# Kernel optimization log

Hardware: AMD Instinct MI355X
Metric: run time of the kernel (lower is better)

Reference implementation:

```python
import jax, jax.numpy as jnp
import numpy as np

TEMPERATURE = 0.07
B, D = 8192, 1024
NUM_CLASSES = 100


def setup_inputs() -> dict:
    key = jax.random.key(0)
    k1, k2 = jax.random.split(key)
    e = jax.random.normal(k1, (B, D), dtype=jnp.float32)
    e = e / jnp.linalg.norm(e, axis=1, keepdims=True)  # module assumes L2-normalized embeds
    labels = jax.random.randint(k2, (B,), 0, NUM_CLASSES)
    return {"embeds": e, "labels": labels}


def reference(embeds, labels):
    # logits[i, j] = <e_i, e_j> / T    (B, B)
    logits = (embeds @ embeds.T) / TEMPERATURE
    same = labels[None, :] == labels[:, None]  # (B, B) symmetric label-match mask
    # denominator: logsumexp over rows i with a DIFFERENT label than column j
    neg_masked = jnp.where(same, -jnp.inf, logits)
    base_denom_row = jax.scipy.special.logsumexp(neg_masked, axis=0)  # (B,)
    # numerator pairs: same label, off-diagonal
    in_numer = same & ~jnp.eye(B, dtype=bool)
    numer_count = in_numer.sum(axis=0)  # (B,) per-column positive count
    # log_denom[i, j] = logaddexp(logits[i, j], base_denom_row[i]) where in_numer
    log_denom = jnp.logaddexp(logits, base_denom_row[:, None])
    ce = jnp.where(in_numer, log_denom - logits, 0.0)  # -(numer - log_denom), 0 elsewhere
    count_safe = jnp.maximum(numer_count, 1).astype(ce.dtype)  # guard (unused cols are all-zero)
    return jnp.sum(ce / count_safe[None, :]) / B
```

## Files before the change

### kernel.cpp

```cpp
#include <hip/hip_runtime.h>
#include <math.h>

#define B 8192
#define D 1024
#define INV_T (1.0f/0.07f)
#define CMAX (1.0f/0.07f)
#define SPLITS 8
#define CW (B/SPLITS)
#define MAXM 256
#define NCLS 100
#define NRB (B/128)
#define NTRI (NRB*(NRB+1)/2)

typedef __attribute__((ext_vector_type(4))) float  f32x4;
typedef __attribute__((ext_vector_type(8))) int    i32x8;

__device__ __forceinline__ int sw02(int x) {
    return (x & 2) | ((x & 1) << 2) | ((x >> 2) & 1);
}

__global__ __launch_bounds__(256) void convert_kernel(const float* __restrict__ E,
                                                      unsigned char* __restrict__ E8) {
    int i = blockIdx.x * 256 + threadIdx.x;
    float4 v = ((const float4*)E)[i];
    int lo = __builtin_amdgcn_cvt_pk_fp8_f32(v.x, v.y, 0, false);
    int pk = __builtin_amdgcn_cvt_pk_fp8_f32(v.z, v.w, lo, true);
    ((int*)E8)[i] = pk;
}

__device__ __forceinline__ void stage_tile8(const unsigned char* __restrict__ E8,
                                            char* As, char* Bs,
                                            int row0, int col0, int k0,
                                            int w, int srow, int sk) {
#pragma unroll
    for (int q = 0; q < 4; ++q) {
        const char* ga = (const char*)(E8 + (size_t)(row0 + srow + q * 8) * D + k0) + sk;
        const char* gb = (const char*)(E8 + (size_t)(col0 + srow + q * 8) * D + k0) + sk;
        __builtin_amdgcn_global_load_lds(
            (const __attribute__((address_space(1))) unsigned int*)ga,
            (__attribute__((address_space(3))) unsigned int*)(As + w * 4096 + q * 1024),
            16, 0, 0);
        __builtin_amdgcn_global_load_lds(
            (const __attribute__((address_space(1))) unsigned int*)gb,
            (__attribute__((address_space(3))) unsigned int*)(Bs + w * 4096 + q * 1024),
            16, 0, 0);
    }
}

__global__ __launch_bounds__(256, 2) void lse_sym_kernel(const unsigned char* __restrict__ E8,
                                                         const int* __restrict__ labels,
                                                         float* __restrict__ part) {
    __shared__ char As[128 * 128];
    __shared__ char Bs[128 * 128];
    __shared__ float sh_r[4][64];
    __shared__ float sh_c[4][64];

    int bid = (blockIdx.x & 7) * (NTRI / 8) + (blockIdx.x >> 3);
    int rb = 0, off = 0;
    while (off + (NRB - rb) <= bid) { off += NRB - rb; ++rb; }
    const int cb = rb + (bid - off);

    const int row0 = rb * 128;
    const int col0 = cb * 128;
    const int t    = threadIdx.x;
    const int lane = t & 63;
    const int w    = t >> 6;
    const int wr   = w >> 1;
    const int wc   = w & 1;

    int rlab[16];
#pragma unroll
    for (int m = 0; m < 4; ++m)
#pragma unroll
        for (int r = 0; r < 4; ++r)
            rlab[m * 4 + r] = labels[row0 + wr * 64 + m * 16 + ((lane >> 4) << 2) + r];
    int clab[4];
#pragma unroll
    for (int n = 0; n < 4; ++n) clab[n] = labels[col0 + wc * 64 + n * 16 + (lane & 15)];

    const int srow = w * 32 + (lane >> 3);
    const int sk   = sw02((lane & 7) ^ (lane >> 3)) << 4;
    const int p    = lane >> 4;
    const int kq   = 2 * (p & 1) + (p >> 1);
    const int swz  = (lane & 7) << 4;
    const int loff = (kq << 4) ^ swz;

    f32x4 acc[4][4];
#pragma unroll
    for (int m = 0; m < 4; ++m)
#pragma unroll
        for (int n = 0; n < 4; ++n) { f32x4 z = {0.f, 0.f, 0.f, 0.f}; acc[m][n] = z; }

    const int nt = D / 128;
    for (int kt = 0; kt < nt; ++kt) {
        __syncthreads();
        stage_tile8(E8, As, Bs, row0, col0, kt * 128, w, srow, sk);
        __syncthreads();

        i32x8 b[4];
#pragma unroll
        for (int n = 0; n < 4; ++n) {
            int row = wc * 64 + n * 16 + (lane & 15);
            const char* pb = Bs + row * 128;
            int4 lo = *(const int4*)(pb + loff);
            int4 hi = *(const int4*)(pb + (loff ^ 64));
            b[n][0] = lo.x; b[n][1] = lo.y; b[n][2] = lo.z; b[n][3] = lo.w;
            b[n][4] = hi.x; b[n][5] = hi.y; b[n][6] = hi.z; b[n][7] = hi.w;
        }

        __builtin_amdgcn_s_setprio(1);
#pragma unroll
        for (int m = 0; m < 4; ++m) {
            int row = wr * 64 + m * 16 + (lane & 15);
            const char* pa = As + row * 128;
            int4 lo = *(const int4*)(pa + loff);
            int4 hi = *(const int4*)(pa + (loff ^ 64));
            i32x8 a;
            a[0] = lo.x; a[1] = lo.y; a[2] = lo.z; a[3] = lo.w;
            a[4] = hi.x; a[5] = hi.y; a[6] = hi.z; a[7] = hi.w;
#pragma unroll
            for (int n = 0; n < 4; ++n)
                acc[m][n] = __builtin_amdgcn_mfma_scale_f32_16x16x128_f8f6f4(
                    a, b[n], acc[m][n], 0, 0, 0, 127, 0, 127);
        }
        __builtin_amdgcn_s_setprio(0);
    }

    float rsum[16];
#pragma unroll
    for (int i = 0; i < 16; ++i) rsum[i] = 0.f;
    float csum[4];
#pragma unroll
    for (int n = 0; n < 4; ++n) csum[n] = 0.f;

#pragma unroll
    for (int m = 0; m < 4; ++m)
#pragma unroll
        for (int n = 0; n < 4; ++n)
#pragma unroll
            for (int r = 0; r < 4; ++r) {
                float x = acc[m][n][r] * INV_T;
                float e = (rlab[m * 4 + r] != clab[n]) ? __expf(x - CMAX) : 0.f;
                rsum[m * 4 + r] += e;
                csum[n] += e;
            }

#pragma unroll
    for (int o = 1; o < 16; o <<= 1)
#pragma unroll
        for (int i = 0; i < 16; ++i) rsum[i] += __shfl_xor(rsum[i], o);
    if ((lane & 15) == 0) {
#pragma unroll
        for (int m = 0; m < 4; ++m)
#pragma unroll
            for (int r = 0; r < 4; ++r)
                sh_r[w][m * 16 + ((lane >> 4) << 2) + r] = rsum[m * 4 + r];
    }
#pragma unroll
    for (int n = 0; n < 4; ++n) {
        csum[n] += __shfl_xor(csum[n], 16);
        csum[n] += __shfl_xor(csum[n], 32);
    }
    if (lane < 16) {
#pragma unroll
        for (int n = 0; n < 4; ++n) sh_c[w][n * 16 + lane] = csum[n];
    }
    __syncthreads();
    if (t < 128) {
        int wri = t >> 6, idx = t & 63;
        float s = sh_r[wri * 2][idx] + sh_r[wri * 2 + 1][idx];
        part[(size_t)(row0 + t) * NRB + cb] = s;
    } else if (rb != cb) {
        int c = t - 128;
        int wci = c >> 6, idx = c & 63;
        float s = sh_c[wci][idx] + sh_c[2 + wci][idx];
        part[(size_t)(col0 + c) * NRB + rb] = s;
    }
}

__global__ __launch_bounds__(256) void combine_kernel(const float* __restrict__ part,
                                                      float* __restrict__ base) {
    int i = blockIdx.x * 256 + threadIdx.x;
    float s = 0.f;
#pragma unroll
    for (int k = 0; k < NRB; ++k) s += part[(size_t)i * NRB + k];
    base[i] = logf(s) + CMAX;
}

__global__ __launch_bounds__(256) void class_list_kernel(const int* __restrict__ labels,
                                                         int* __restrict__ members,
                                                         int* __restrict__ cnt) {
    const int c = blockIdx.x;
    const int tt = threadIdx.x;
    const int lane = tt & 63, w = tt >> 6;
    __shared__ int wcnt[4];
    int cw = 0;
    for (int b0 = w * 2048; b0 < (w + 1) * 2048; b0 += 64)
        cw += __popcll(__ballot(labels[b0 + lane] == c));
    if (lane == 0) wcnt[w] = cw;
    __syncthreads();
    int cum = 0;
    for (int x = 0; x < w; ++x) cum += wcnt[x];
    for (int b0 = w * 2048; b0 < (w + 1) * 2048; b0 += 64) {
        bool match = (labels[b0 + lane] == c);
        unsigned long long mask = __ballot(match);
        int pre = __popcll(mask & ((1ull << lane) - 1ull));
        if (match) members[c * MAXM + cum + pre] = b0 + lane;
        cum += __popcll(mask);
    }
    if (tt == 0) cnt[c] = wcnt[0] + wcnt[1] + wcnt[2] + wcnt[3];
}

__global__ __launch_bounds__(256) void numer_mfma_kernel(const unsigned char* __restrict__ E8,
                                                         const float* __restrict__ base,
                                                         const int* __restrict__ members,
                                                         const int* __restrict__ cnt,
                                                         float* __restrict__ part2) {
    const int c  = blockIdx.x;
    const int rt = blockIdx.y;
    const int ctile = blockIdx.z;
    const int t    = threadIdx.x;
    const int lane = t & 63;
    const int w    = t >> 6;
    const int n    = cnt[c];
    const int pidx = c * 16 + rt * 4 + ctile;

    __shared__ char As[64 * 128];
    __shared__ char Bs[64 * 128];
    __shared__ float red[256];

    if (rt * 64 >= n || ctile * 64 >= n) {
        if (t == 0) part2[pidx] = 0.f;
        return;
    }

    int gi[4]; float bi[4]; bool iv[4];
#pragma unroll
    for (int r = 0; r < 4; ++r) {
        int il = rt * 64 + w * 16 + ((lane >> 4) << 2) + r;
        iv[r] = (il < n);
        int idx = members[c * MAXM + (iv[r] ? il : 0)];
        gi[r] = il;
        bi[r] = base[idx];
    }
    int gj[4]; bool jv[4];
#pragma unroll
    for (int nn = 0; nn < 4; ++nn) {
        int jl = ctile * 64 + nn * 16 + (lane & 15);
        jv[nn] = (jl < n);
        gj[nn] = jl;
    }

    const int lr   = (lane >> 3);
    const int sk   = sw02((lane & 7) ^ lr) << 4;
    const int pp   = lane >> 4;
    const int kq   = 2 * (pp & 1) + (pp >> 1);
    const int swz  = (lane & 7) << 4;
    const int loff = (kq << 4) ^ swz;

    int arow[2], brow[2];
#pragma unroll
    for (int q = 0; q < 2; ++q) {
        int al = rt * 64 + w * 16 + q * 8 + lr;
        int bl = ctile * 64 + w * 16 + q * 8 + lr;
        arow[q] = members[c * MAXM + ((al < n) ? al : 0)];
        brow[q] = members[c * MAXM + ((bl < n) ? bl : 0)];
    }

    f32x4 acc[4];
#pragma unroll
    for (int nn = 0; nn < 4; ++nn) { f32x4 z = {0.f, 0.f, 0.f, 0.f}; acc[nn] = z; }

    for (int kt = 0; kt < D / 128; ++kt) {
        __syncthreads();
#pragma unroll
        for (int q = 0; q < 2; ++q) {
            const char* ga = (const char*)(E8 + (size_t)arow[q] * D + kt * 128) + sk;
            const char* gb = (const char*)(E8 + (size_t)brow[q] * D + kt * 128) + sk;
            __builtin_amdgcn_global_load_lds(
                (const __attribute__((address_space(1))) unsigned int*)ga,
                (__attribute__((address_space(3))) unsigned int*)(As + w * 2048 + q * 1024),
                16, 0, 0);
            __builtin_amdgcn_global_load_lds(
                (const __attribute__((address_space(1))) unsigned int*)gb,
                (__attribute__((address_space(3))) unsigned int*)(Bs + w * 2048 + q * 1024),
                16, 0, 0);
        }
        __syncthreads();

        i32x8 a, b[4];
        {
            int row = w * 16 + (lane & 15);
            const char* pa = As + row * 128;
            int4 lo = *(const int4*)(pa + loff);
            int4 hi = *(const int4*)(pa + (loff ^ 64));
            a[0] = lo.x; a[1] = lo.y; a[2] = lo.z; a[3] = lo.w;
            a[4] = hi.x; a[5] = hi.y; a[6] = hi.z; a[7] = hi.w;
        }
#pragma unroll
        for (int nn = 0; nn < 4; ++nn) {
            int row = nn * 16 + (lane & 15);
            const char* pb = Bs + row * 128;
            int4 lo = *(const int4*)(pb + loff);
            int4 hi = *(const int4*)(pb + (loff ^ 64));
            b[nn][0] = lo.x; b[nn][1] = lo.y; b[nn][2] = lo.z; b[nn][3] = lo.w;
            b[nn][4] = hi.x; b[nn][5] = hi.y; b[nn][6] = hi.z; b[nn][7] = hi.w;
        }
#pragma unroll
        for (int nn = 0; nn < 4; ++nn)
            acc[nn] = __builtin_amdgcn_mfma_scale_f32_16x16x128_f8f6f4(
                a, b[nn], acc[nn], 0, 0, 0, 127, 0, 127);
    }

    float psum = 0.f;
#pragma unroll
    for (int nn = 0; nn < 4; ++nn)
#pragma unroll
        for (int r = 0; r < 4; ++r) {
            if (iv[r] && jv[nn] && gi[r] != gj[nn]) {
                float x = bi[r] - acc[nn][r] * INV_T;
                psum += (x > 15.f) ? x : log1pf(__expf(x));
            }
        }
    red[t] = psum;
    __syncthreads();
    for (int g = 128; g > 0; g >>= 1) {
        if (t < g) red[t] += red[t + g];
        __syncthreads();
    }
    if (t == 0) part2[pidx] = red[0];
}

__global__ __launch_bounds__(256) void final2_kernel(const float* __restrict__ part2,
                                                     const int* __restrict__ cnt,
                                                     float* __restrict__ out) {
    __shared__ float red[256];
    int t = threadIdx.x;
    float acc = 0.f;
    for (int p = t; p < NCLS * 16; p += 256) {
        int c = p >> 4;
        float wgt = (cnt[c] > 1) ? 1.f / (float)(cnt[c] - 1) : 0.f;
        acc += part2[p] * wgt;
    }
    red[t] = acc;
    __syncthreads();
    for (int g = 128; g > 0; g >>= 1) {
        if (t < g) red[t] += red[t + g];
        __syncthreads();
    }
    if (t == 0) out[0] = red[0] / (float)B;
}

#define BR 64
#define BC 64
#define KT 32
#define PAD 68
__global__ __launch_bounds__(256) void lse_f32_kernel(const float* __restrict__ E,
                                                      const int* __restrict__ labels,
                                                      float2* __restrict__ part) {
    __shared__ float As[KT][PAD];
    __shared__ float Bs[KT][PAD];
    __shared__ int   clabs[BC];
    __shared__ float msh[BR][16];
    __shared__ float ssh[BR][16];
    const int rb = blockIdx.x, cs = blockIdx.y;
    const int row0 = rb * BR;
    const int t = threadIdx.x;
    const int tx = t & 15, ty = t >> 4;
    int rlab[4];
#pragma unroll
    for (int i = 0; i < 4; ++i) rlab[i] = labels[row0 + ty * 4 + i];
    float m[4], s[4];
#pragma unroll
    for (int i = 0; i < 4; ++i) { m[i] = -INFINITY; s[i] = 0.f; }
    for (int ct = 0; ct < CW / BC; ++ct) {
        const int col0 = cs * CW + ct * BC;
        __syncthreads();
        if (t < BC) clabs[t] = labels[col0 + t];
        float acc[4][4];
#pragma unroll
        for (int i = 0; i < 4; ++i)
#pragma unroll
            for (int j = 0; j < 4; ++j) acc[i][j] = 0.f;
        for (int k0 = 0; k0 < D; k0 += KT) {
            __syncthreads();
#pragma unroll
            for (int q = 0; q < 2; ++q) {
                int id = q * 256 + t, row = id >> 3, kk = (id & 7) * 4;
                float4 va = *(const float4*)&E[(size_t)(row0 + row) * D + k0 + kk];
                As[kk + 0][row] = va.x; As[kk + 1][row] = va.y;
                As[kk + 2][row] = va.z; As[kk + 3][row] = va.w;
                float4 vb = *(const float4*)&E[(size_t)(col0 + row) * D + k0 + kk];
                Bs[kk + 0][row] = vb.x; Bs[kk + 1][row] = vb.y;
                Bs[kk + 2][row] = vb.z; Bs[kk + 3][row] = vb.w;
            }
            __syncthreads();
#pragma unroll
            for (int kk = 0; kk < KT; ++kk) {
                float4 av = *(const float4*)&As[kk][ty * 4];
                float4 bv = *(const float4*)&Bs[kk][tx * 4];
                float a_[4] = {av.x, av.y, av.z, av.w};
                float b_[4] = {bv.x, bv.y, bv.z, bv.w};
#pragma unroll
                for (int i = 0; i < 4; ++i)
#pragma unroll
                    for (int j = 0; j < 4; ++j) acc[i][j] += a_[i] * b_[j];
            }
        }
#pragma unroll
        for (int j = 0; j < 4; ++j) {
            int cl = clabs[tx * 4 + j];
#pragma unroll
            for (int i = 0; i < 4; ++i) {
                if (rlab[i] != cl) {
                    float x = acc[i][j] * INV_T;
                    if (x > m[i]) { s[i] = s[i] * __expf(m[i] - x) + 1.f; m[i] = x; }
                    else           s[i] += __expf(x - m[i]);
                }
            }
        }
    }
    __syncthreads();
#pragma unroll
    for (int i = 0; i < 4; ++i) { msh[ty * 4 + i][tx] = m[i]; ssh[ty * 4 + i][tx] = s[i]; }
    __syncthreads();
    if (t < BR) {
        float M = -INFINITY, S = 0.f;
#pragma unroll
        for (int x = 0; x < 16; ++x) {
            float pm = msh[t][x], ps = ssh[t][x];
            if (pm > M)             { S = S * __expf(M - pm) + ps; M = pm; }
            else if (pm > -INFINITY)  S += ps * __expf(pm - M);
        }
        part[(size_t)(row0 + t) * SPLITS + cs] = make_float2(M, S);
    }
}
__global__ __launch_bounds__(256) void combine_f32_kernel(const float2* __restrict__ part,
                                                          float* __restrict__ base) {
    int i = blockIdx.x * 256 + threadIdx.x;
    if (i >= B) return;
    float M = -INFINITY, S = 0.f;
#pragma unroll
    for (int k = 0; k < SPLITS; ++k) {
        float2 p = part[(size_t)i * SPLITS + k];
        if (p.x > M)             { S = S * __expf(M - p.x) + p.y; M = p.x; }
        else if (p.x > -INFINITY)  S += p.y * __expf(p.x - M);
    }
    base[i] = M + logf(S);
}
__global__ __launch_bounds__(256) void numer_kernel(const float* __restrict__ E,
                                                    const int* __restrict__ labels,
                                                    const float* __restrict__ base,
                                                    const int* __restrict__ members,
                                                    const int* __restrict__ cnt,
                                                    float* __restrict__ rowpart) {
    const int i = blockIdx.x;
    const int t = threadIdx.x;
    const int lane = t & 63, w = t >> 6;
    __shared__ float ei[D];
    __shared__ float wacc[4];
    ((float4*)ei)[t] = ((const float4*)(E + (size_t)i * D))[t];
    const int   li = labels[i];
    const float bi = base[i];
    const int   n  = cnt[li];
    __syncthreads();
    float acc = 0.f;
    const float4* U = (const float4*)ei;
    for (int s = w; s < n; s += 4) {
        int j = members[li * MAXM + s];
        if (j == i) continue;
        const float4* Ej = (const float4*)(E + (size_t)j * D);
        float d = 0.f;
#pragma unroll
        for (int q = 0; q < 4; ++q) {
            float4 v = Ej[lane + 64 * q];
            float4 u = U[lane + 64 * q];
            d += v.x * u.x + v.y * u.y + v.z * u.z + v.w * u.w;
        }
#pragma unroll
        for (int o = 32; o > 0; o >>= 1) d += __shfl_xor(d, o);
        if (lane == 0) {
            float x = bi - d * INV_T;
            acc += (x > 15.f) ? x : log1pf(__expf(x));
        }
    }
    if (lane == 0) wacc[w] = acc;
    __syncthreads();
    if (t == 0) {
        float a = wacc[0] + wacc[1] + wacc[2] + wacc[3];
        rowpart[i] = (n > 1) ? a / (float)(n - 1) : 0.f;
    }
}
__global__ __launch_bounds__(256) void final_kernel(const float* __restrict__ rowpart,
                                                    float* __restrict__ out) {
    __shared__ float red[256];
    int t = threadIdx.x;
    float acc = 0.f;
    for (int k = 0; k < B / 256; ++k) acc += rowpart[t + k * 256];
    red[t] = acc;
    __syncthreads();
    for (int g = 128; g > 0; g >>= 1) {
        if (t < g) red[t] += red[t + g];
        __syncthreads();
    }
    if (t == 0) out[0] = red[0] / (float)B;
}

extern "C" void kernel_launch(void* const* d_in, const int* in_sizes, int n_in,
                              void* d_out, int out_size, void* d_ws, size_t ws_size,
                              hipStream_t stream) {
    const float* E      = (const float*)d_in[0];
    const int*   labels = (const int*)d_in[1];
    float*       out    = (float*)d_out;

    const size_t szE8   = (size_t)B * D;
    const size_t szPart = (size_t)B * NRB * 4;
    const size_t need   = szE8 + szPart + 4 * B + 4 * B + 4 * NCLS * MAXM
                        + 4 * NCLS + 4 * NCLS * 16 + 512;

    if (ws_size >= need) {
        char* ws = (char*)d_ws;
        unsigned char* E8 = (unsigned char*)ws;  ws += szE8;
        float* part    = (float*)ws;   ws += szPart;
        float* base    = (float*)ws;   ws += 4 * B;
        float* rowpart = (float*)ws;   ws += 4 * B;   (void)rowpart;
        int*   members = (int*)ws;     ws += 4 * NCLS * MAXM;
        int*   cnt     = (int*)ws;     ws += 4 * NCLS;
        float* part2   = (float*)ws;

        convert_kernel<<<B * D / 4 / 256, 256, 0, stream>>>(E, E8);
        lse_sym_kernel<<<NTRI, 256, 0, stream>>>(E8, labels, part);
        combine_kernel<<<B / 256, 256, 0, stream>>>(part, base);
        class_list_kernel<<<NCLS, 256, 0, stream>>>(labels, members, cnt);
        numer_mfma_kernel<<<dim3(NCLS, 4, 4), 256, 0, stream>>>(E8, base, members, cnt, part2);
        final2_kernel<<<1, 256, 0, stream>>>(part2, cnt, out);
    } else {
        char* ws = (char*)d_ws;
        float2* part   = (float2*)ws;  ws += sizeof(float2) * B * SPLITS;
        float* base    = (float*)ws;   ws += 4 * B;
        float* rowpart = (float*)ws;   ws += 4 * B;
        int*   members = (int*)ws;     ws += 4 * NCLS * MAXM;
        int*   cnt     = (int*)ws;

        lse_f32_kernel<<<dim3(B / BR, SPLITS), 256, 0, stream>>>(E, labels, part);
        combine_f32_kernel<<<B / 256, 256, 0, stream>>>(part, base);
        class_list_kernel<<<NCLS, 256, 0, stream>>>(labels, members, cnt);
        numer_kernel<<<B, 256, 0, stream>>>(E, labels, base, members, cnt, rowpart);
        final_kernel<<<1, 256, 0, stream>>>(rowpart, out);
    }
}
```

Baseline: 97.69 us.

## Load MFMA operands directly from global memory instead of staging through LDS

Removes the LDS staging of A and B tiles, along with the two barriers per k-step and the priority hints. Each lane now reads its fp8 operand fragments straight from global memory using per-row pointers. This removes synchronization and LDS traffic, but each wave re-fetches data that other waves share. It also relies on cache hit rates and exposes global latency with no software pipelining.

New measurement: 182.1 us. +86.4%, slower.

```diff
diff --git a/kernel.cpp b/kernel.cpp
--- a/kernel.cpp
+++ b/kernel.cpp
@@ -28,30 +28,9 @@
     ((int*)E8)[i] = pk;
 }
 
-__device__ __forceinline__ void stage_tile8(const unsigned char* __restrict__ E8,
-                                            char* As, char* Bs,
-                                            int row0, int col0, int k0,
-                                            int w, int srow, int sk) {
-#pragma unroll
-    for (int q = 0; q < 4; ++q) {
-        const char* ga = (const char*)(E8 + (size_t)(row0 + srow + q * 8) * D + k0) + sk;
-        const char* gb = (const char*)(E8 + (size_t)(col0 + srow + q * 8) * D + k0) + sk;
-        __builtin_amdgcn_global_load_lds(
-            (const __attribute__((address_space(1))) unsigned int*)ga,
-            (__attribute__((address_space(3))) unsigned int*)(As + w * 4096 + q * 1024),
-            16, 0, 0);
-        __builtin_amdgcn_global_load_lds(
-            (const __attribute__((address_space(1))) unsigned int*)gb,
-            (__attribute__((address_space(3))) unsigned int*)(Bs + w * 4096 + q * 1024),
-            16, 0, 0);
-    }
-}
-
 __global__ __launch_bounds__(256, 2) void lse_sym_kernel(const unsigned char* __restrict__ E8,
                                                          const int* __restrict__ labels,
                                                          float* __restrict__ part) {
-    __shared__ char As[128 * 128];
-    __shared__ char Bs[128 * 128];
     __shared__ float sh_r[4][64];
     __shared__ float sh_c[4][64];
 
@@ -78,12 +57,16 @@
 #pragma unroll
     for (int n = 0; n < 4; ++n) clab[n] = labels[col0 + wc * 64 + n * 16 + (lane & 15)];
 
-    const int srow = w * 32 + (lane >> 3);
-    const int sk   = sw02((lane & 7) ^ (lane >> 3)) << 4;
-    const int p    = lane >> 4;
-    const int kq   = 2 * (p & 1) + (p >> 1);
-    const int swz  = (lane & 7) << 4;
-    const int loff = (kq << 4) ^ swz;
+    const unsigned char* Arow[4];
+    const unsigned char* Brow[4];
+#pragma unroll
+    for (int m = 0; m < 4; ++m)
+        Arow[m] = E8 + (size_t)(row0 + wr * 64 + m * 16 + (lane & 15)) * D;
+#pragma unroll
+    for (int n = 0; n < 4; ++n)
+        Brow[n] = E8 + (size_t)(col0 + wc * 64 + n * 16 + (lane & 15)) * D;
+
+    const int kq = (lane >> 4) << 5;
 
     f32x4 acc[4][4];
 #pragma unroll
@@ -93,28 +76,20 @@
 
     const int nt = D / 128;
     for (int kt = 0; kt < nt; ++kt) {
-        __syncthreads();
-        stage_tile8(E8, As, Bs, row0, col0, kt * 128, w, srow, sk);
-        __syncthreads();
+        const int ko = kt * 128 + kq;
 
         i32x8 b[4];
 #pragma unroll
         for (int n = 0; n < 4; ++n) {
-            int row = wc * 64 + n * 16 + (lane & 15);
-            const char* pb = Bs + row * 128;
-            int4 lo = *(const int4*)(pb + loff);
-            int4 hi = *(const int4*)(pb + (loff ^ 64));
+            int4 lo = *(const int4*)(Brow[n] + ko);
+            int4 hi = *(const int4*)(Brow[n] + ko + 16);
             b[n][0] = lo.x; b[n][1] = lo.y; b[n][2] = lo.z; b[n][3] = lo.w;
             b[n][4] = hi.x; b[n][5] = hi.y; b[n][6] = hi.z; b[n][7] = hi.w;
         }
-
-        __builtin_amdgcn_s_setprio(1);
 #pragma unroll
         for (int m = 0; m < 4; ++m) {
-            int row = wr * 64 + m * 16 + (lane & 15);
-            const char* pa = As + row * 128;
-            int4 lo = *(const int4*)(pa + loff);
-            int4 hi = *(const int4*)(pa + (loff ^ 64));
+            int4 lo = *(const int4*)(Arow[m] + ko);
+            int4 hi = *(const int4*)(Arow[m] + ko + 16);
             i32x8 a;
             a[0] = lo.x; a[1] = lo.y; a[2] = lo.z; a[3] = lo.w;
             a[4] = hi.x; a[5] = hi.y; a[6] = hi.z; a[7] = hi.w;
@@ -123,7 +98,6 @@
                 acc[m][n] = __builtin_amdgcn_mfma_scale_f32_16x16x128_f8f6f4(
                     a, b[n], acc[m][n], 0, 0, 0, 127, 0, 127);
         }
-        __builtin_amdgcn_s_setprio(0);
     }
 
     float rsum[16];
```
